# Kernel tuning notes

Measured on AMD Instinct MI355X. Metric: run time of the kernel, lower is better.

## Reference

```python
import jax, jax.numpy as jnp
import numpy as np

N = 262144
HIDDEN = 512
NUM_GATES = 64
NUM_GRAPHS = 1024
EPS = 1e-16


def setup_inputs() -> dict:
    key = jax.random.key(0)
    k1, k2, k3 = jax.random.split(key, 3)
    x = jax.random.normal(k1, (N, HIDDEN), dtype=jnp.float32)
    batch = jnp.sort(jax.random.randint(k2, (N,), 0, NUM_GRAPHS, dtype=jnp.int64))
    # Xavier-uniform init for the gate weight [hidden, num_gates]
    limit = float(np.sqrt(6.0 / (HIDDEN + NUM_GATES)))
    W = jax.random.uniform(k3, (HIDDEN, NUM_GATES), dtype=jnp.float32,
                           minval=-limit, maxval=limit)
    return {"x": x, "batch": batch, "W": W}


def _segment_softmax(gate, batch, num_segments):
    # Numerically-stable softmax within each segment (per gate column).
    seg_max = jax.ops.segment_max(gate, batch, num_segments=num_segments)  # [G, num_gates]
    gate = jnp.exp(gate - seg_max[batch])
    seg_sum = jax.ops.segment_sum(gate, batch, num_segments=num_segments)  # [G, num_gates]
    return gate / (seg_sum[batch] + EPS)


def reference(x, batch, W):
    # gate = x @ W : [N, num_gates]
    gate = x @ W
    gate = _segment_softmax(gate, batch, NUM_GRAPHS)
    # weighted scatter-add pooling: out[g] = sum_{i in g} mean_k(gate[i,k]) * x[i]
    weights = jnp.mean(gate, axis=-1, keepdims=True)  # [N, 1]
    out = jax.ops.segment_sum(weights * x, batch, num_segments=NUM_GRAPHS)  # [G, hidden]
    return out
```

## Files before the change

kernel.cpp:

```cpp
#include <hip/hip_runtime.h>

#define NROWS   262144
#define HIDDEN  512
#define NGATES  64
#define NGRAPHS 1024
#define MAXR    512

typedef __attribute__((ext_vector_type(8))) short short8;
typedef __attribute__((ext_vector_type(4))) float floatx4;

__device__ __forceinline__ unsigned short f2bf(float f) {
    unsigned int u = __float_as_uint(f);
    unsigned int r = (u + 0x7fffu + ((u >> 16) & 1u)) >> 16;
    return (unsigned short)r;
}
__device__ __forceinline__ float bf2f(unsigned short u) {
    return __uint_as_float((unsigned int)u << 16);
}

__global__ void k_wfrag(const float* __restrict__ W, unsigned short* __restrict__ wf) {
    int tile = blockIdx.x;
    int lane = threadIdx.x;
    int kstep = tile >> 2, nt = tile & 3;
    int kbase = kstep * 32 + (lane >> 4) * 8;
    int col   = nt * 16 + (lane & 15);
    unsigned short* dst = wf + ((size_t)tile * 64 + lane) * 8;
#pragma unroll
    for (int j = 0; j < 8; ++j)
        dst[j] = f2bf(W[(size_t)(kbase + j) * NGATES + col]);
}

__global__ void k_bounds(const int* __restrict__ batch, int* __restrict__ segstart) {
    int g = blockIdx.x * blockDim.x + threadIdx.x;
    if (g > NGRAPHS) return;
    if (g == NGRAPHS) { segstart[g] = NROWS; return; }
    int lo = 0, hi = NROWS;
    while (lo < hi) { int mid = (lo + hi) >> 1; if (batch[mid] < g) lo = mid + 1; else hi = mid; }
    segstart[g] = lo;
}

__global__ __launch_bounds__(1024, 4) void k_main(const float* __restrict__ x,
                                                  const unsigned short* __restrict__ wf,
                                                  const int* __restrict__ segstart,
                                                  float* __restrict__ out) {
    __shared__ unsigned short eL[MAXR * NGATES];
    __shared__ float wl[MAXR];
    __shared__ float sums[NGATES];
    __shared__ float rinv[NGATES];

    const int g = blockIdx.x;
    const int t = threadIdx.x;
    const int lane = t & 63, wv = t >> 6;
    const int m = lane & 15, q = lane >> 4;
    const int s = segstart[g], e = segstart[g + 1];
    const int rows = min(e - s, MAXR);
    const int tiles = (rows + 15) >> 4;

    if (t < NGATES) sums[t] = 0.f;
    __syncthreads();

    const short8* wfv = (const short8*)wf;
    float vs0 = 0.f, vs1 = 0.f, vs2 = 0.f, vs3 = 0.f;

    for (int tile = wv; tile < tiles; tile += 16) {
        const int garow = s + tile * 16 + m;
        const float* xrow = x + (size_t)min(garow, NROWS - 1) * HIDDEN + q * 8;

        floatx4 acc0 = {0.f,0.f,0.f,0.f}, acc1 = {0.f,0.f,0.f,0.f};
        floatx4 acc2 = {0.f,0.f,0.f,0.f}, acc3 = {0.f,0.f,0.f,0.f};
#pragma unroll 4
        for (int ks = 0; ks < 16; ++ks) {
            float4 a0 = *(const float4*)(xrow + ks * 32);
            float4 a1 = *(const float4*)(xrow + ks * 32 + 4);
            short8 af;
            af[0] = (short)f2bf(a0.x); af[1] = (short)f2bf(a0.y);
            af[2] = (short)f2bf(a0.z); af[3] = (short)f2bf(a0.w);
            af[4] = (short)f2bf(a1.x); af[5] = (short)f2bf(a1.y);
            af[6] = (short)f2bf(a1.z); af[7] = (short)f2bf(a1.w);
            short8 b0 = wfv[(ks * 4 + 0) * 64 + lane];
            short8 b1 = wfv[(ks * 4 + 1) * 64 + lane];
            short8 b2 = wfv[(ks * 4 + 2) * 64 + lane];
            short8 b3 = wfv[(ks * 4 + 3) * 64 + lane];
            acc0 = __builtin_amdgcn_mfma_f32_16x16x32_bf16(af, b0, acc0, 0, 0, 0);
            acc1 = __builtin_amdgcn_mfma_f32_16x16x32_bf16(af, b1, acc1, 0, 0, 0);
            acc2 = __builtin_amdgcn_mfma_f32_16x16x32_bf16(af, b2, acc2, 0, 0, 0);
            acc3 = __builtin_amdgcn_mfma_f32_16x16x32_bf16(af, b3, acc3, 0, 0, 0);
        }

        const int rl0 = tile * 16 + q * 4;
#pragma unroll
        for (int r = 0; r < 4; ++r) {
            const int rloc = rl0 + r;
            const bool valid = rloc < rows;
            const float e0 = valid ? __expf(acc0[r]) : 0.f;
            const float e1 = valid ? __expf(acc1[r]) : 0.f;
            const float e2 = valid ? __expf(acc2[r]) : 0.f;
            const float e3 = valid ? __expf(acc3[r]) : 0.f;
            if (valid) {
                unsigned short* eb = eL + rloc * NGATES + m;
                eb[ 0] = f2bf(e0); eb[16] = f2bf(e1);
                eb[32] = f2bf(e2); eb[48] = f2bf(e3);
            }
            vs0 += e0; vs1 += e1; vs2 += e2; vs3 += e3;
        }
    }
    vs0 += __shfl_xor(vs0, 16, 64); vs0 += __shfl_xor(vs0, 32, 64);
    vs1 += __shfl_xor(vs1, 16, 64); vs1 += __shfl_xor(vs1, 32, 64);
    vs2 += __shfl_xor(vs2, 16, 64); vs2 += __shfl_xor(vs2, 32, 64);
    vs3 += __shfl_xor(vs3, 16, 64); vs3 += __shfl_xor(vs3, 32, 64);
    if (q == 0) {
        atomicAdd(&sums[m],      vs0); atomicAdd(&sums[m + 16], vs1);
        atomicAdd(&sums[m + 32], vs2); atomicAdd(&sums[m + 48], vs3);
    }
    __syncthreads();
    if (t < NGATES) rinv[t] = 1.0f / (sums[t] + 1e-16f);
    __syncthreads();

    const float rk = rinv[lane];
    const int nrq = (rows + 3) >> 2;
    for (int i4 = wv; i4 < nrq; i4 += 16) {
        const int rb = i4 * 4;
        float v0 = bf2f(eL[(rb + 0) * NGATES + lane]) * rk;
        float v1 = bf2f(eL[(rb + 1) * NGATES + lane]) * rk;
        float v2 = bf2f(eL[(rb + 2) * NGATES + lane]) * rk;
        float v3 = bf2f(eL[(rb + 3) * NGATES + lane]) * rk;
#pragma unroll
        for (int off = 1; off < 64; off <<= 1) {
            v0 += __shfl_xor(v0, off, 64);
            v1 += __shfl_xor(v1, off, 64);
            v2 += __shfl_xor(v2, off, 64);
            v3 += __shfl_xor(v3, off, 64);
        }
        if (lane == 0) {
            wl[rb + 0] = v0 * (1.0f / 64.0f); wl[rb + 1] = v1 * (1.0f / 64.0f);
            wl[rb + 2] = v2 * (1.0f / 64.0f); wl[rb + 3] = v3 * (1.0f / 64.0f);
        }
    }
    __syncthreads();

    const int h2 = (t & 255) * 2;
    const int p = t >> 8;
    float ax = 0.f, ay = 0.f;
#pragma unroll 4
    for (int i = p; i < rows; i += 4) {
        const float w = wl[i];
        const float2 xv = *(const float2*)(x + (size_t)(s + i) * HIDDEN + h2);
        ax = fmaf(w, xv.x, ax);
        ay = fmaf(w, xv.y, ay);
    }
    float* red = (float*)eL;
    red[(p * 256 + (t & 255)) * 2 + 0] = ax;
    red[(p * 256 + (t & 255)) * 2 + 1] = ay;
    __syncthreads();
    if (p == 0) {
        const int c = (t & 255) * 2;
        float2 o;
        o.x = red[c]     + red[512 + c]     + red[1024 + c]     + red[1536 + c];
        o.y = red[c + 1] + red[512 + c + 1] + red[1024 + c + 1] + red[1536 + c + 1];
        *(float2*)(out + (size_t)g * HIDDEN + h2) = o;
    }
}

extern "C" void kernel_launch(void* const* d_in, const int* in_sizes, int n_in,
                              void* d_out, int out_size, void* d_ws, size_t ws_size,
                              hipStream_t stream) {
    const float* x     = (const float*)d_in[0];
    const int*   batch = (const int*)d_in[1];
    const float* W     = (const float*)d_in[2];
    float* out = (float*)d_out;

    unsigned short* wfrag = (unsigned short*)d_ws;
    int* segstart = (int*)((char*)d_ws + (64 << 10));

    hipLaunchKernelGGL(k_wfrag, dim3(64), dim3(64), 0, stream, W, wfrag);
    hipLaunchKernelGGL(k_bounds, dim3(5), dim3(256), 0, stream, batch, segstart);
    hipLaunchKernelGGL(k_main, dim3(NGRAPHS), dim3(1024), 0, stream, x, wfrag, segstart, out);
}
```

Before: 775.8 us.

## Pipeline gate and pooling phases over row chunks with MFMA pooling

Each block now handles four graphs, split into 128-row chunks. Gate computation for the next chunk is software-pipelined against pooling of the current chunk through double-buffered transposed exp tiles in LDS. Pooling becomes an MFMA product of exp weights with x, using a hi/lo bf16 split of x to keep precision, and the softmax normalisation and gate mean are applied once per graph at the end. This removes the per-row shuffle reductions and the large per-graph LDS buffer. In exchange it doubles the pooling MFMA work, re-reads x with scalar per-lane loads, and gives the grid fewer blocks.

```diff
diff --git a/kernel.cpp b/kernel.cpp
--- a/kernel.cpp
+++ b/kernel.cpp
@@ -5,6 +5,9 @@
 #define NGATES  64
 #define NGRAPHS 1024
 #define MAXR    512
+#define CH      128
+#define ETS     136
+#define GPB     4
 
 typedef __attribute__((ext_vector_type(8))) short short8;
 typedef __attribute__((ext_vector_type(4))) float floatx4;
@@ -43,27 +46,47 @@
                                                   const unsigned short* __restrict__ wf,
                                                   const int* __restrict__ segstart,
                                                   float* __restrict__ out) {
-    __shared__ unsigned short eL[MAXR * NGATES];
-    __shared__ float wl[MAXR];
-    __shared__ float sums[NGATES];
+    __shared__ unsigned short eT[2][NGATES][ETS];
+    __shared__ float sums[2][NGATES];
     __shared__ float rinv[NGATES];
 
-    const int g = blockIdx.x;
     const int t = threadIdx.x;
     const int lane = t & 63, wv = t >> 6;
     const int m = lane & 15, q = lane >> 4;
-    const int s = segstart[g], e = segstart[g + 1];
-    const int rows = min(e - s, MAXR);
-    const int tiles = (rows + 15) >> 4;
-
-    if (t < NGATES) sums[t] = 0.f;
-    __syncthreads();
+    const int G0 = blockIdx.x * GPB;
+
+    int sg[GPB + 1];
+#pragma unroll
+    for (int k = 0; k <= GPB; ++k) sg[k] = segstart[G0 + k];
+    const int r0 = min(sg[1] - sg[0], MAXR), r1 = min(sg[2] - sg[1], MAXR);
+    const int r2 = min(sg[3] - sg[2], MAXR), r3 = min(sg[4] - sg[3], MAXR);
+    const int n0 = max(1, (r0 + CH - 1) / CH), n1 = max(1, (r1 + CH - 1) / CH);
+    const int n2 = max(1, (r2 + CH - 1) / CH), n3 = max(1, (r3 + CH - 1) / CH);
+    const int p1 = n0, p2 = n0 + n1, p3 = n0 + n1 + n2;
+    const int nitems = n0 + n1 + n2 + n3;
+
+    auto decode = [&](int j, int& chbase, int& chrows, int& par, bool& lastc) {
+        int gi = (j >= p1) + (j >= p2) + (j >= p3);
+        int pstart = gi == 0 ? 0 : (gi == 1 ? p1 : (gi == 2 ? p2 : p3));
+        int sbase  = gi == 0 ? sg[0] : (gi == 1 ? sg[1] : (gi == 2 ? sg[2] : sg[3]));
+        int rowsg  = gi == 0 ? r0 : (gi == 1 ? r1 : (gi == 2 ? r2 : r3));
+        int nchg   = gi == 0 ? n0 : (gi == 1 ? n1 : (gi == 2 ? n2 : n3));
+        int ch = j - pstart;
+        chbase = sbase + ch * CH;
+        chrows = min(rowsg - ch * CH, CH);
+        par = gi & 1;
+        lastc = (ch == nchg - 1);
+    };
 
     const short8* wfv = (const short8*)wf;
-    float vs0 = 0.f, vs1 = 0.f, vs2 = 0.f, vs3 = 0.f;
-
-    for (int tile = wv; tile < tiles; tile += 16) {
-        const int garow = s + tile * 16 + m;
+
+    auto gate_phase = [&](int j) {
+        if (wv >= 8) return;
+        int chbase, chrows, par; bool lastc;
+        decode(j, chbase, chrows, par, lastc);
+        const int buf = j & 1;
+        const int rloc0 = wv * 16;
+        const int garow = chbase + rloc0 + m;
         const float* xrow = x + (size_t)min(garow, NROWS - 1) * HIDDEN + q * 8;
 
         floatx4 acc0 = {0.f,0.f,0.f,0.f}, acc1 = {0.f,0.f,0.f,0.f};
@@ -87,77 +110,120 @@
             acc3 = __builtin_amdgcn_mfma_f32_16x16x32_bf16(af, b3, acc3, 0, 0, 0);
         }
 
-        const int rl0 = tile * 16 + q * 4;
+        float vs0 = 0.f, vs1 = 0.f, vs2 = 0.f, vs3 = 0.f;
+        unsigned short pe[4][4];
 #pragma unroll
         for (int r = 0; r < 4; ++r) {
-            const int rloc = rl0 + r;
-            const bool valid = rloc < rows;
+            const int rloc = rloc0 + q * 4 + r;
+            const bool valid = rloc < chrows;
             const float e0 = valid ? __expf(acc0[r]) : 0.f;
             const float e1 = valid ? __expf(acc1[r]) : 0.f;
             const float e2 = valid ? __expf(acc2[r]) : 0.f;
             const float e3 = valid ? __expf(acc3[r]) : 0.f;
-            if (valid) {
-                unsigned short* eb = eL + rloc * NGATES + m;
-                eb[ 0] = f2bf(e0); eb[16] = f2bf(e1);
-                eb[32] = f2bf(e2); eb[48] = f2bf(e3);
+            pe[0][r] = f2bf(e0); pe[1][r] = f2bf(e1);
+            pe[2][r] = f2bf(e2); pe[3][r] = f2bf(e3);
+            vs0 += e0; vs1 += e1; vs2 += e2; vs3 += e3;
+        }
+#pragma unroll
+        for (int nt = 0; nt < 4; ++nt) {
+            ushort4 pk; pk.x = pe[nt][0]; pk.y = pe[nt][1]; pk.z = pe[nt][2]; pk.w = pe[nt][3];
+            *(ushort4*)&eT[buf][nt * 16 + m][rloc0 + q * 4] = pk;
+        }
+        vs0 += __shfl_xor(vs0, 16, 64); vs0 += __shfl_xor(vs0, 32, 64);
+        vs1 += __shfl_xor(vs1, 16, 64); vs1 += __shfl_xor(vs1, 32, 64);
+        vs2 += __shfl_xor(vs2, 16, 64); vs2 += __shfl_xor(vs2, 32, 64);
+        vs3 += __shfl_xor(vs3, 16, 64); vs3 += __shfl_xor(vs3, 32, 64);
+        if (q == 0) {
+            atomicAdd(&sums[par][m],      vs0); atomicAdd(&sums[par][m + 16], vs1);
+            atomicAdd(&sums[par][m + 32], vs2); atomicAdd(&sums[par][m + 48], vs3);
+        }
+    };
+
+    floatx4 D00={0.f,0.f,0.f,0.f}, D01={0.f,0.f,0.f,0.f}, D10={0.f,0.f,0.f,0.f}, D11={0.f,0.f,0.f,0.f};
+    floatx4 D20={0.f,0.f,0.f,0.f}, D21={0.f,0.f,0.f,0.f}, D30={0.f,0.f,0.f,0.f}, D31={0.f,0.f,0.f,0.f};
+
+    auto pool_phase = [&](int j) {
+        int chbase, chrows, par; bool lastc;
+        decode(j, chbase, chrows, par, lastc);
+        const int buf = j & 1;
+        const int c0 = wv * 32;
+#pragma unroll
+        for (int ks2 = 0; ks2 < 4; ++ks2) {
+            const int rowb = chbase + ks2 * 32 + q * 8;
+            short8 bh0, bl0, bh1, bl1;
+#pragma unroll
+            for (int jj = 0; jj < 8; ++jj) {
+                const int rr = min(rowb + jj, NROWS - 1);
+                const float v0 = x[(size_t)rr * HIDDEN + c0 + m];
+                const float v1 = x[(size_t)rr * HIDDEN + c0 + 16 + m];
+                const unsigned short h0 = f2bf(v0);
+                const unsigned short h1 = f2bf(v1);
+                bh0[jj] = (short)h0; bl0[jj] = (short)f2bf(v0 - bf2f(h0));
+                bh1[jj] = (short)h1; bl1[jj] = (short)f2bf(v1 - bf2f(h1));
             }
-            vs0 += e0; vs1 += e1; vs2 += e2; vs3 += e3;
-        }
-    }
-    vs0 += __shfl_xor(vs0, 16, 64); vs0 += __shfl_xor(vs0, 32, 64);
-    vs1 += __shfl_xor(vs1, 16, 64); vs1 += __shfl_xor(vs1, 32, 64);
-    vs2 += __shfl_xor(vs2, 16, 64); vs2 += __shfl_xor(vs2, 32, 64);
-    vs3 += __shfl_xor(vs3, 16, 64); vs3 += __shfl_xor(vs3, 32, 64);
-    if (q == 0) {
-        atomicAdd(&sums[m],      vs0); atomicAdd(&sums[m + 16], vs1);
-        atomicAdd(&sums[m + 32], vs2); atomicAdd(&sums[m + 48], vs3);
-    }
+            const short8 a0 = *(const short8*)&eT[buf][ 0 + m][ks2 * 32 + q * 8];
+            const short8 a1 = *(const short8*)&eT[buf][16 + m][ks2 * 32 + q * 8];
+            const short8 a2 = *(const short8*)&eT[buf][32 + m][ks2 * 32 + q * 8];
+            const short8 a3 = *(const short8*)&eT[buf][48 + m][ks2 * 32 + q * 8];
+            D00 = __builtin_amdgcn_mfma_f32_16x16x32_bf16(a0, bh0, D00, 0, 0, 0);
+            D00 = __builtin_amdgcn_mfma_f32_16x16x32_bf16(a0, bl0, D00, 0, 0, 0);
+            D01 = __builtin_amdgcn_mfma_f32_16x16x32_bf16(a0, bh1, D01, 0, 0, 0);
+            D01 = __builtin_amdgcn_mfma_f32_16x16x32_bf16(a0, bl1, D01, 0, 0, 0);
+            D10 = __builtin_amdgcn_mfma_f32_16x16x32_bf16(a1, bh0, D10, 0, 0, 0);
+            D10 = __builtin_amdgcn_mfma_f32_16x16x32_bf16(a1, bl0, D10, 0, 0, 0);
+            D11 = __builtin_amdgcn_mfma_f32_16x16x32_bf16(a1, bh1, D11, 0, 0, 0);
+            D11 = __builtin_amdgcn_mfma_f32_16x16x32_bf16(a1, bl1, D11, 0, 0, 0);
+            D20 = __builtin_amdgcn_mfma_f32_16x16x32_bf16(a2, bh0, D20, 0, 0, 0);
+            D20 = __builtin_amdgcn_mfma_f32_16x16x32_bf16(a2, bl0, D20, 0, 0, 0);
+            D21 = __builtin_amdgcn_mfma_f32_16x16x32_bf16(a2, bh1, D21, 0, 0, 0);
+            D21 = __builtin_amdgcn_mfma_f32_16x16x32_bf16(a2, bl1, D21, 0, 0, 0);
+            D30 = __builtin_amdgcn_mfma_f32_16x16x32_bf16(a3, bh0, D30, 0, 0, 0);
+            D30 = __builtin_amdgcn_mfma_f32_16x16x32_bf16(a3, bl0, D30, 0, 0, 0);
+            D31 = __builtin_amdgcn_mfma_f32_16x16x32_bf16(a3, bh1, D31, 0, 0, 0);
+            D31 = __builtin_amdgcn_mfma_f32_16x16x32_bf16(a3, bl1, D31, 0, 0, 0);
+        }
+    };
+
+    if (t < 2 * NGATES) ((float*)sums)[t] = 0.f;
     __syncthreads();
-    if (t < NGATES) rinv[t] = 1.0f / (sums[t] + 1e-16f);
+    gate_phase(0);
     __syncthreads();
 
-    const float rk = rinv[lane];
-    const int nrq = (rows + 3) >> 2;
-    for (int i4 = wv; i4 < nrq; i4 += 16) {
-        const int rb = i4 * 4;
-        float v0 = bf2f(eL[(rb + 0) * NGATES + lane]) * rk;
-        float v1 = bf2f(eL[(rb + 1) * NGATES + lane]) * rk;
-        float v2 = bf2f(eL[(rb + 2) * NGATES + lane]) * rk;
-        float v3 = bf2f(eL[(rb + 3) * NGATES + lane]) * rk;
-#pragma unroll
-        for (int off = 1; off < 64; off <<= 1) {
-            v0 += __shfl_xor(v0, off, 64);
-            v1 += __shfl_xor(v1, off, 64);
-            v2 += __shfl_xor(v2, off, 64);
-            v3 += __shfl_xor(v3, off, 64);
-        }
-        if (lane == 0) {
-            wl[rb + 0] = v0 * (1.0f / 64.0f); wl[rb + 1] = v1 * (1.0f / 64.0f);
-            wl[rb + 2] = v2 * (1.0f / 64.0f); wl[rb + 3] = v3 * (1.0f / 64.0f);
-        }
-    }
-    __syncthreads();
-
-    const int h2 = (t & 255) * 2;
-    const int p = t >> 8;
-    float ax = 0.f, ay = 0.f;
-#pragma unroll 4
-    for (int i = p; i < rows; i += 4) {
-        const float w = wl[i];
-        const float2 xv = *(const float2*)(x + (size_t)(s + i) * HIDDEN + h2);
-        ax = fmaf(w, xv.x, ax);
-        ay = fmaf(w, xv.y, ay);
-    }
-    float* red = (float*)eL;
-    red[(p * 256 + (t & 255)) * 2 + 0] = ax;
-    red[(p * 256 + (t & 255)) * 2 + 1] = ay;
-    __syncthreads();
-    if (p == 0) {
-        const int c = (t & 255) * 2;
-        float2 o;
-        o.x = red[c]     + red[512 + c]     + red[1024 + c]     + red[1536 + c];
-        o.y = red[c + 1] + red[512 + c + 1] + red[1024 + c + 1] + red[1536 + c + 1];
-        *(float2*)(out + (size_t)g * HIDDEN + h2) = o;
+    for (int i = 0; i < nitems; ++i) {
+        if (i + 1 < nitems) gate_phase(i + 1);
+        pool_phase(i);
+
+        int chbase, chrows, par; bool lastc;
+        decode(i, chbase, chrows, par, lastc);
+        if (lastc) {
+            __syncthreads();
+            if (t < NGATES) rinv[t] = 1.0f / (sums[par][t] + 1e-16f);
+            __syncthreads();
+            const int gi = (i >= p1) + (i >= p2) + (i >= p3);
+            const int c0 = wv * 32;
+            float cs0 = 0.f, cs1 = 0.f;
+#pragma unroll
+            for (int r = 0; r < 4; ++r) {
+                const float rv0 = rinv[ 0 + q * 4 + r];
+                const float rv1 = rinv[16 + q * 4 + r];
+                const float rv2 = rinv[32 + q * 4 + r];
+                const float rv3 = rinv[48 + q * 4 + r];
+                cs0 += D00[r] * rv0 + D10[r] * rv1 + D20[r] * rv2 + D30[r] * rv3;
+                cs1 += D01[r] * rv0 + D11[r] * rv1 + D21[r] * rv2 + D31[r] * rv3;
+            }
+            cs0 += __shfl_xor(cs0, 16, 64); cs0 += __shfl_xor(cs0, 32, 64);
+            cs1 += __shfl_xor(cs1, 16, 64); cs1 += __shfl_xor(cs1, 32, 64);
+            if (q == 0) {
+                out[(size_t)(G0 + gi) * HIDDEN + c0 + m]      = cs0 * (1.0f / 64.0f);
+                out[(size_t)(G0 + gi) * HIDDEN + c0 + 16 + m] = cs1 * (1.0f / 64.0f);
+            }
+            D00 = (floatx4){0.f,0.f,0.f,0.f}; D01 = (floatx4){0.f,0.f,0.f,0.f};
+            D10 = (floatx4){0.f,0.f,0.f,0.f}; D11 = (floatx4){0.f,0.f,0.f,0.f};
+            D20 = (floatx4){0.f,0.f,0.f,0.f}; D21 = (floatx4){0.f,0.f,0.f,0.f};
+            D30 = (floatx4){0.f,0.f,0.f,0.f}; D31 = (floatx4){0.f,0.f,0.f,0.f};
+            if (t < NGATES) sums[par][t] = 0.f;
+        }
+        __syncthreads();
     }
 }
 
@@ -174,5 +240,5 @@
 
     hipLaunchKernelGGL(k_wfrag, dim3(64), dim3(64), 0, stream, W, wfrag);
     hipLaunchKernelGGL(k_bounds, dim3(5), dim3(256), 0, stream, batch, segstart);
-    hipLaunchKernelGGL(k_main, dim3(NGRAPHS), dim3(1024), 0, stream, x, wfrag, segstart, out);
-}
+    hipLaunchKernelGGL(k_main, dim3(NGRAPHS / GPB), dim3(1024), 0, stream, x, wfrag, segstart, out);
+}
```

Result: slower. 886.0 us (+14.2%).
